# Optimization experiments

Hardware: AMD Instinct MI355X
Metric: run time of the kernel (lower is better)

## Reference

```python
import jax, jax.numpy as jnp
import numpy as np
from jax import lax

THRESHOLD = 0.5
KERNEL_SIZE = 4

# OpenCV morphologyEx(MORPH_OPEN) = erosion followed by dilation.
# For an even ksize k=4 with default anchor (-1,-1) -> anchor=(2,2):
#   erosion window offsets  = [-2, +1]  -> pad (2, 1)
#   dilation (kernel mirrored) offsets = [-1, +2] -> pad (1, 2)

def _erode(m, k):
    return lax.reduce_window(m, jnp.inf, lax.min,
                             window_dimensions=(1, k, k),
                             window_strides=(1, 1, 1),
                             padding=((0, 0), (k // 2, k - 1 - k // 2), (k // 2, k - 1 - k // 2)))

def _dilate(m, k):
    return lax.reduce_window(m, -jnp.inf, lax.max,
                             window_dimensions=(1, k, k),
                             window_strides=(1, 1, 1),
                             padding=((0, 0), (k - 1 - k // 2, k // 2), (k - 1 - k // 2, k // 2)))

def setup_inputs() -> dict:
    key = jax.random.key(0)
    k1, k2 = jax.random.split(key)
    score = jax.random.uniform(k1, (32, 1000), dtype=jnp.float32)
    mask = jax.random.uniform(k2, (32, 1024, 1024), dtype=jnp.float32)
    return {"score": score, "mask": mask}

def reference(score, mask):
    score = jnp.where(THRESHOLD <= score, score, jnp.zeros((), score.dtype))
    mask = jnp.where(THRESHOLD <= mask, mask, jnp.zeros((), mask.dtype))
    mask = _dilate(_erode(mask, KERNEL_SIZE), KERNEL_SIZE)  # morphological opening
    return (score, mask)
```

## Files before the change

### kernel.cpp

```cpp
#include <hip/hip_runtime.h>
#include <math.h>


#define H 1024
#define W 1024
#define R 16
#define STRIPS (H / R)
#define SEGS 4
#define BATCH 32
#define TASKS (STRIPS * SEGS * BATCH)
#define MASK_BLOCKS (TASKS / 4)
#define N_SCORE 32000
#define SCORE_BLOCKS ((N_SCORE + 255) / 256)
#define ITERS (R + 6)

__device__ __forceinline__ float th(float v) { return v >= 0.5f ? v : 0.0f; }

__global__ __launch_bounds__(256)
__attribute__((amdgpu_waves_per_eu(4, 4)))
void fused_kernel(const float* __restrict__ score,
                  const float* __restrict__ mask,
                  float* __restrict__ out) {
    const int bid0 = blockIdx.x;
    const int tid  = threadIdx.x;

    if (bid0 < SCORE_BLOCKS) {
        int i = bid0 * 256 + tid;
        if (i < N_SCORE) out[i] = th(score[i]);
        return;
    }
    const int mb0 = bid0 - SCORE_BLOCKS;

    const int bid = (mb0 & 7) * (MASK_BLOCKS / 8) + (mb0 >> 3);

    const int wave = tid >> 6;
    const int lane = tid & 63;
    const int task = bid * 4 + wave;
    const int b    = task >> 8;
    const int rem  = task & 255;
    const int strip= rem >> 2;
    const int seg  = rem & 3;
    const int y0   = strip * R;
    const int c0   = seg * 256 + lane * 4;

    const float* img  = mask + (size_t)b * (H * W);
    float*       outp = out + N_SCORE + (size_t)b * (H * W);

    const bool eL = (c0 == 0);
    const bool eR = (c0 == W - 4);
    const bool sm = (lane == 0) || (lane == 63);
    const int oS = (lane == 0) ? (eL ? 0 : c0 - 4)
                               : (eR ? W - 4 : c0 + 4);

    float4 own[3], seam[3];

#define ISSUE(IT) do {                                                   \
        int t_  = y0 - 3 + (IT);                                         \
        int tc_ = t_ < 0 ? 0 : (t_ >= H ? H - 1 : t_);      \
        const float* row_ = img + (size_t)tc_ * W;                       \
        own[(IT) % 3] = *(const float4*)(row_ + c0);                     \
        if (sm) seam[(IT) % 3] = *(const float4*)(row_ + oS);            \
    } while (0)

    ISSUE(0); ISSUE(1); ISSUE(2);

    float hmP[7], q1[7], q2[7];
    #pragma unroll
    for (int m = 0; m < 7; ++m) { hmP[m] = q1[m] = q2[m] = INFINITY; }
    float hxP[4], u1[4], u2[4];
    #pragma unroll
    for (int j = 0; j < 4; ++j)  { hxP[j] = u1[j] = u2[j] = -INFINITY; }

    #pragma unroll
    for (int it = 0; it < ITERS; ++it) {
        const int t   = y0 - 3 + it;
        const int buf = it % 3;
        const bool rowOK = (t >= 0) && (t < H);

        float4 ow = own[buf];
        float4 sw = seam[buf];
        float a0 = __shfl_up(ow.y, 1);
        float a1 = __shfl_up(ow.z, 1);
        float a2 = __shfl_up(ow.w, 1);
        float a7 = __shfl_down(ow.x, 1);
        float a8 = __shfl_down(ow.y, 1);
        float a9 = __shfl_down(ow.z, 1);
        a0 = (lane == 0)  ? sw.y : a0;
        a1 = (lane == 0)  ? sw.z : a1;
        a2 = (lane == 0)  ? sw.w : a2;
        a7 = (lane == 63) ? sw.x : a7;
        a8 = (lane == 63) ? sw.y : a8;
        a9 = (lane == 63) ? sw.z : a9;
        float ar[10];
        ar[0] = eL ? INFINITY : a0;
        ar[1] = eL ? INFINITY : a1;
        ar[2] = eL ? INFINITY : a2;
        ar[3] = ow.x;  ar[4] = ow.y;  ar[5] = ow.z;  ar[6] = ow.w;
        ar[7] = eR ? INFINITY : a7;
        ar[8] = eR ? INFINITY : a8;
        ar[9] = eR ? INFINITY : a9;

        if (it + 3 < ITERS) ISSUE(it + 3);

        float p[9];
        #pragma unroll
        for (int m = 0; m < 9; ++m) p[m] = fminf(ar[m], ar[m + 1]);
        float hm[7];
        #pragma unroll
        for (int m = 0; m < 7; ++m) {
            float v = fminf(p[m], p[m + 2]);
            hm[m] = rowOK ? v : INFINITY;
        }

        const int r = t - 1;
        const float rlim = (r >= 0 && r < H) ? INFINITY : -INFINITY;
        float qt[7], ec[7];
        #pragma unroll
        for (int m = 0; m < 7; ++m) {
            qt[m] = fminf(hmP[m], hm[m]);
            ec[m] = fminf(fminf(qt[m], q2[m]), rlim);
        }
        ec[0] = eL ? -INFINITY : ec[0];
        ec[5] = eR ? -INFINITY : ec[5];
        ec[6] = eR ? -INFINITY : ec[6];

        #pragma unroll
        for (int m = 0; m < 7; ++m) { q2[m] = q1[m]; q1[m] = qt[m]; hmP[m] = hm[m]; }

        float p2[6];
        #pragma unroll
        for (int j = 0; j < 6; ++j) p2[j] = fmaxf(ec[j], ec[j + 1]);
        float hx[4], ur[4];
        #pragma unroll
        for (int j = 0; j < 4; ++j) {
            hx[j] = fmaxf(p2[j], p2[j + 2]);
            ur[j] = fmaxf(hxP[j], hx[j]);
        }

        if (it >= 6) {
            const int y = t - 3;
            float o[4];
            #pragma unroll
            for (int j = 0; j < 4; ++j)
                o[j] = th(fmaxf(ur[j], u2[j]));
            float* po = outp + (size_t)y * W + c0;
            *(float4*)(po) = make_float4(o[0], o[1], o[2], o[3]);
        }

        #pragma unroll
        for (int j = 0; j < 4; ++j) { u2[j] = u1[j]; u1[j] = ur[j]; hxP[j] = hx[j]; }
    }
#undef ISSUE
}

extern "C" void kernel_launch(void* const* d_in, const int* in_sizes, int n_in,
                              void* d_out, int out_size, void* d_ws, size_t ws_size,
                              hipStream_t stream) {
    const float* score = (const float*)d_in[0];
    const float* mask  = (const float*)d_in[1];
    float* out = (float*)d_out;

    const int grid = MASK_BLOCKS + SCORE_BLOCKS;
    fused_kernel<<<grid, 256, 0, stream>>>(score, mask, out);
}
```

Baseline: 265.1 us.

## Stage full image rows through LDS via direct global-to-LDS loads

Each block now processes a whole 1024-wide row strip, with its four waves spanning the row instead of four independent segments. Rows are staged into a 4-slot LDS ring buffer with padded infinity borders using global_load_lds, replacing the cross-lane shuffles and extra seam loads. Manual vmcnt waits and a block barrier per row step keep the pipeline two rows ahead. The waves_per_eu attribute is removed. In exchange, every row step now pays a workgroup barrier and relies on hand-computed vmcnt counts that must match the number of outstanding stores and loads.

```diff
diff --git a/kernel.cpp b/kernel.cpp
--- a/kernel.cpp
+++ b/kernel.cpp
@@ -6,18 +6,17 @@
 #define W 1024
 #define R 16
 #define STRIPS (H / R)
-#define SEGS 4
 #define BATCH 32
-#define TASKS (STRIPS * SEGS * BATCH)
-#define MASK_BLOCKS (TASKS / 4)
+#define MASK_BLOCKS (STRIPS * BATCH)
 #define N_SCORE 32000
 #define SCORE_BLOCKS ((N_SCORE + 255) / 256)
 #define ITERS (R + 6)
+#define LROW 1032
+#define NSLOT 4
 
 __device__ __forceinline__ float th(float v) { return v >= 0.5f ? v : 0.0f; }
 
 __global__ __launch_bounds__(256)
-__attribute__((amdgpu_waves_per_eu(4, 4)))
 void fused_kernel(const float* __restrict__ score,
                   const float* __restrict__ mask,
                   float* __restrict__ out) {
@@ -30,127 +29,109 @@
         return;
     }
     const int mb0 = bid0 - SCORE_BLOCKS;
-
     const int bid = (mb0 & 7) * (MASK_BLOCKS / 8) + (mb0 >> 3);
 
-    const int wave = tid >> 6;
-    const int lane = tid & 63;
-    const int task = bid * 4 + wave;
-    const int b    = task >> 8;
-    const int rem  = task & 255;
-    const int strip= rem >> 2;
-    const int seg  = rem & 3;
-    const int y0   = strip * R;
-    const int c0   = seg * 256 + lane * 4;
+    const int b     = bid >> 6;
+    const int strip = bid & 63;
+    const int y0    = strip * R;
+    const int wave  = tid >> 6;
+    const int c0    = tid * 4;
 
     const float* img  = mask + (size_t)b * (H * W);
     float*       outp = out + N_SCORE + (size_t)b * (H * W);
 
-    const bool eL = (c0 == 0);
-    const bool eR = (c0 == W - 4);
-    const bool sm = (lane == 0) || (lane == 63);
-    const int oS = (lane == 0) ? (eL ? 0 : c0 - 4)
-                               : (eR ? W - 4 : c0 + 4);
+    __shared__ float smem[NSLOT * LROW];
 
-    float4 own[3], seam[3];
+    if (tid < 8 * NSLOT) {
+        int s = tid >> 3, k = tid & 7;
+        smem[s * LROW + (k < 4 ? k : 1024 + k)] = INFINITY;
+    }
+    __syncthreads();
 
-#define ISSUE(IT) do {                                                   \
-        int t_  = y0 - 3 + (IT);                                         \
-        int tc_ = t_ < 0 ? 0 : (t_ >= H ? H - 1 : t_);      \
-        const float* row_ = img + (size_t)tc_ * W;                       \
-        own[(IT) % 3] = *(const float4*)(row_ + c0);                     \
-        if (sm) seam[(IT) % 3] = *(const float4*)(row_ + oS);            \
+    const bool eL = (tid == 0);
+    const bool eR = (tid == 255);
+
+#define STAGE(IT) do {                                                        \
+        int t_  = y0 - 3 + (IT);                                              \
+        int tc_ = t_ < 0 ? 0 : (t_ > H - 1 ? H - 1 : t_);        \
+        const float* gsrc = img + (size_t)tc_ * W + c0;         \
+        float* ldst = &smem[((IT) & 3) * LROW + 4 + (wave << 8)];  \
+        __builtin_amdgcn_global_load_lds(                                     \
+            (const __attribute__((address_space(1))) void*)gsrc,              \
+            (__attribute__((address_space(3))) void*)ldst, 16, 0, 0);         \
     } while (0)
 
-    ISSUE(0); ISSUE(1); ISSUE(2);
-
     float hmP[7], q1[7], q2[7];
-    #pragma unroll
     for (int m = 0; m < 7; ++m) { hmP[m] = q1[m] = q2[m] = INFINITY; }
     float hxP[4], u1[4], u2[4];
-    #pragma unroll
     for (int j = 0; j < 4; ++j)  { hxP[j] = u1[j] = u2[j] = -INFINITY; }
 
-    #pragma unroll
-    for (int it = 0; it < ITERS; ++it) {
-        const int t   = y0 - 3 + it;
-        const int buf = it % 3;
-        const bool rowOK = (t >= 0) && (t < H);
+    STAGE(0); STAGE(1);
 
-        float4 ow = own[buf];
-        float4 sw = seam[buf];
-        float a0 = __shfl_up(ow.y, 1);
-        float a1 = __shfl_up(ow.z, 1);
-        float a2 = __shfl_up(ow.w, 1);
-        float a7 = __shfl_down(ow.x, 1);
-        float a8 = __shfl_down(ow.y, 1);
-        float a9 = __shfl_down(ow.z, 1);
-        a0 = (lane == 0)  ? sw.y : a0;
-        a1 = (lane == 0)  ? sw.z : a1;
-        a2 = (lane == 0)  ? sw.w : a2;
-        a7 = (lane == 63) ? sw.x : a7;
-        a8 = (lane == 63) ? sw.y : a8;
-        a9 = (lane == 63) ? sw.z : a9;
-        float ar[10];
-        ar[0] = eL ? INFINITY : a0;
-        ar[1] = eL ? INFINITY : a1;
-        ar[2] = eL ? INFINITY : a2;
-        ar[3] = ow.x;  ar[4] = ow.y;  ar[5] = ow.z;  ar[6] = ow.w;
-        ar[7] = eR ? INFINITY : a7;
-        ar[8] = eR ? INFINITY : a8;
-        ar[9] = eR ? INFINITY : a9;
+#define STEP(IT) do {                                                         \
+        if ((IT) + 2 < ITERS) STAGE((IT) + 2);                                \
+        { constexpr int K_ = ((IT) + 1 < ITERS ? 1 : 0)                       \
+                           + ((IT) + 2 < ITERS ? 1 : 0)                       \
+                           + ((IT) >= 7 ? 1 : 0) + ((IT) >= 8 ? 1 : 0);       \
+          asm volatile("s_waitcnt vmcnt(%0)" :: "i"(K_) : "memory"); }        \
+        __builtin_amdgcn_s_barrier();                                         \
+        __builtin_amdgcn_sched_barrier(0);                                    \
+        {                                                                     \
+            const int t = y0 - 3 + (IT);                                      \
+            const bool rowOK = (t >= 0) && (t < H);              \
+            const float* ls = &smem[((IT) & 3) * LROW + c0];                  \
+            float4 L0 = *(const float4*)(ls);            \
+            float4 L1 = *(const float4*)(ls + 4);        \
+            float4 L2 = *(const float4*)(ls + 8);        \
+            float ar[10];                                                     \
+            ar[0] = L0.y; ar[1] = L0.z; ar[2] = L0.w;                         \
+            ar[3] = L1.x; ar[4] = L1.y; ar[5] = L1.z; ar[6] = L1.w;           \
+            ar[7] = L2.x; ar[8] = L2.y; ar[9] = L2.z;                         \
+            float p[9];                                                       \
+            for (int m = 0; m < 9; ++m) p[m] = fminf(ar[m], ar[m + 1]);       \
+            float hm[7];                                                      \
+            for (int m = 0; m < 7; ++m) {                                     \
+                float v = fminf(p[m], p[m + 2]);                              \
+                hm[m] = rowOK ? v : INFINITY;            \
+            }                                                                 \
+            const int r = t - 1;                                              \
+            const float rlim = (r >= 0 && r < H) ? INFINITY : -INFINITY;      \
+            float qt[7], ec[7];                                               \
+            for (int m = 0; m < 7; ++m) {                                     \
+                qt[m] = fminf(hmP[m], hm[m]);                                 \
+                ec[m] = fminf(fminf(qt[m], q2[m]), rlim);                     \
+            }                                                                 \
+            ec[0] = eL ? -INFINITY : ec[0];             \
+            ec[5] = eR ? -INFINITY : ec[5];             \
+            ec[6] = eR ? -INFINITY : ec[6];             \
+            for (int m = 0; m < 7; ++m) { q2[m] = q1[m]; q1[m] = qt[m]; hmP[m] = hm[m]; } \
+            float p2[6];                                                      \
+            for (int j = 0; j < 6; ++j) p2[j] = fmaxf(ec[j], ec[j + 1]);      \
+            float hx[4], ur[4];                                               \
+            for (int j = 0; j < 4; ++j) {                                     \
+                hx[j] = fmaxf(p2[j], p2[j + 2]);                              \
+                ur[j] = fmaxf(hxP[j], hx[j]);                                 \
+            }                                                                 \
+            if ((IT) >= 6) {                                                  \
+                const int y = t - 3;                                          \
+                float o0 = th(fmaxf(ur[0], u2[0]));                           \
+                float o1 = th(fmaxf(ur[1], u2[1]));                           \
+                float o2 = th(fmaxf(ur[2], u2[2]));                           \
+                float o3 = th(fmaxf(ur[3], u2[3]));                           \
+                *(float4*)(outp + (size_t)y * W + c0) =                       \
+                    make_float4(o0, o1, o2, o3);                              \
+            }                                                                 \
+            for (int j = 0; j < 4; ++j) { u2[j] = u1[j]; u1[j] = ur[j]; hxP[j] = hx[j]; } \
+        }                                                                     \
+    } while (0)
 
-        if (it + 3 < ITERS) ISSUE(it + 3);
+    STEP(0);  STEP(1);  STEP(2);  STEP(3);  STEP(4);  STEP(5);
+    STEP(6);  STEP(7);  STEP(8);  STEP(9);  STEP(10); STEP(11);
+    STEP(12); STEP(13); STEP(14); STEP(15); STEP(16); STEP(17);
+    STEP(18); STEP(19); STEP(20); STEP(21);
 
-        float p[9];
-        #pragma unroll
-        for (int m = 0; m < 9; ++m) p[m] = fminf(ar[m], ar[m + 1]);
-        float hm[7];
-        #pragma unroll
-        for (int m = 0; m < 7; ++m) {
-            float v = fminf(p[m], p[m + 2]);
-            hm[m] = rowOK ? v : INFINITY;
-        }
-
-        const int r = t - 1;
-        const float rlim = (r >= 0 && r < H) ? INFINITY : -INFINITY;
-        float qt[7], ec[7];
-        #pragma unroll
-        for (int m = 0; m < 7; ++m) {
-            qt[m] = fminf(hmP[m], hm[m]);
-            ec[m] = fminf(fminf(qt[m], q2[m]), rlim);
-        }
-        ec[0] = eL ? -INFINITY : ec[0];
-        ec[5] = eR ? -INFINITY : ec[5];
-        ec[6] = eR ? -INFINITY : ec[6];
-
-        #pragma unroll
-        for (int m = 0; m < 7; ++m) { q2[m] = q1[m]; q1[m] = qt[m]; hmP[m] = hm[m]; }
-
-        float p2[6];
-        #pragma unroll
-        for (int j = 0; j < 6; ++j) p2[j] = fmaxf(ec[j], ec[j + 1]);
-        float hx[4], ur[4];
-        #pragma unroll
-        for (int j = 0; j < 4; ++j) {
-            hx[j] = fmaxf(p2[j], p2[j + 2]);
-            ur[j] = fmaxf(hxP[j], hx[j]);
-        }
-
-        if (it >= 6) {
-            const int y = t - 3;
-            float o[4];
-            #pragma unroll
-            for (int j = 0; j < 4; ++j)
-                o[j] = th(fmaxf(ur[j], u2[j]));
-            float* po = outp + (size_t)y * W + c0;
-            *(float4*)(po) = make_float4(o[0], o[1], o[2], o[3]);
-        }
-
-        #pragma unroll
-        for (int j = 0; j < 4; ++j) { u2[j] = u1[j]; u1[j] = ur[j]; hxP[j] = hx[j]; }
-    }
-#undef ISSUE
+#undef STEP
+#undef STAGE
 }
 
 extern "C" void kernel_launch(void* const* d_in, const int* in_sizes, int n_in,
```

Result: faster. 248.9 us (-6.1%).
